# Kernel tuning notes

Measured on AMD Instinct MI355X. Metric: run time of the kernel, lower is better.

Reference implementation:

```python
import jax, jax.numpy as jnp
import numpy as np

B, C, T, H = 2, 1024, 2048, 16
D = C // H  # head dim = 64
SCALE = 1.0 / np.sqrt(D)
NEG_INF = jnp.float32(-1e30)


def setup_inputs() -> dict:
    key = jax.random.key(0)
    ks = jax.random.split(key, 10)
    x = jax.random.normal(ks[0], (B, C, T), dtype=jnp.float32)
    mask = jax.random.randint(ks[1], (B, 1, T), 0, 2).astype(bool)
    mask = mask.at[:, :, 0].set(True)  # avoid all-masked rows -> NaN softmax
    w = 1.0 / np.sqrt(C)
    Wq = jax.random.normal(ks[2], (C, C), dtype=jnp.float32) * w
    bq = jax.random.normal(ks[3], (C,), dtype=jnp.float32) * 0.01
    Wk = jax.random.normal(ks[4], (C, C), dtype=jnp.float32) * w
    bk = jax.random.normal(ks[5], (C,), dtype=jnp.float32) * 0.01
    Wv = jax.random.normal(ks[6], (C, C), dtype=jnp.float32) * w
    bv = jax.random.normal(ks[7], (C,), dtype=jnp.float32) * 0.01
    Wp = jax.random.normal(ks[8], (C, C), dtype=jnp.float32) * w
    bp = jax.random.normal(ks[9], (C,), dtype=jnp.float32) * 0.01
    return {"x": x, "mask": mask, "Wq": Wq, "bq": bq, "Wk": Wk, "bk": bk,
            "Wv": Wv, "bv": bv, "Wp": Wp, "bp": bp}


def _proj(W, b, x):
    # Conv1d with kernel_size=1: per-timestep linear on [B, C, T]
    return jnp.einsum('oc,bct->bot', W, x) + b[:, None]


def _heads(y):
    # [B, C, T] -> [B, H, T, D]
    return y.reshape(B, H, D, T).transpose(0, 1, 3, 2)


def reference(x, mask, Wq, bq, Wk, bk, Wv, bv, Wp, bp):
    q = _heads(_proj(Wq, bq, x))  # [B,H,T,D]
    k = _heads(_proj(Wk, bk, x))
    v = _heads(_proj(Wv, bv, x))
    att = jnp.einsum('bhqd,bhkd->bhqk', q * SCALE, k)  # [B,H,T,T]
    att = jnp.where(mask[:, :, None, :], att, NEG_INF)  # mask keys
    att = jax.nn.softmax(att, axis=-1)
    vm = v * mask[:, :, :, None].astype(v.dtype)  # zero masked values
    out = jnp.einsum('bhqk,bhkd->bhqd', att, vm)  # [B,H,T,D]
    out = out.transpose(0, 1, 3, 2).reshape(B, C, T)
    out = _proj(Wp, bp, out) * mask.astype(x.dtype)  # [B,C,T]
    return (out, mask)
```

## Files before the change

kernel.cpp:

```cpp
#include <hip/hip_runtime.h>
#include <hip/hip_bf16.h>
#include <math.h>

#define BB 2
#define CC 1024
#define TT 2048
#define HH 16
#define DD 64

using short8   = __attribute__((ext_vector_type(8))) short;
using floatx4  = __attribute__((ext_vector_type(4))) float;
using floatx16 = __attribute__((ext_vector_type(16))) float;
using uint2v   = __attribute__((ext_vector_type(2))) unsigned int;
typedef unsigned short ushort_t;

#define MFMA(a, b, c) __builtin_amdgcn_mfma_f32_16x16x32_bf16((a), (b), (c), 0, 0, 0)
#define MFMA32(a, b, c) __builtin_amdgcn_mfma_f32_32x32x16_bf16((a), (b), (c), 0, 0, 0)

#define QSC 0.18033688011112042f

#define PMAGIC   8404857.0f
#define PZERO_BF 0.97265625f

__device__ __forceinline__ ushort_t f2bf(float f) {
    unsigned int u = __float_as_uint(f);
    u += 0x7FFFu + ((u >> 16) & 1u);
    return (ushort_t)(u >> 16);
}
__device__ __forceinline__ float bf2f(ushort_t h) {
    return __uint_as_float(((unsigned int)h) << 16);
}
__device__ __forceinline__ ushort_t f2bf_t(float f) {
    return (ushort_t)(__float_as_uint(f) >> 16);
}
__device__ __forceinline__ unsigned int packtrunc(float a, float b) {
    return __builtin_amdgcn_perm(__float_as_uint(b), __float_as_uint(a),
                                 0x07060302u);
}
__device__ __forceinline__ unsigned int pack2bf_exp(float s0, float s1) {
    float f0 = fmaf(s0, 128.0f, PMAGIC);
    float f1 = fmaf(s1, 128.0f, PMAGIC);
    return __builtin_amdgcn_perm(__float_as_uint(f1), __float_as_uint(f0),
                                 0x05040100u);
}
__device__ __forceinline__ void load_lds16(const void* g, void* s) {
    __builtin_amdgcn_global_load_lds(
        (const __attribute__((address_space(1))) void*)g,
        (__attribute__((address_space(3))) void*)s, 16, 0, 0);
}

static constexpr size_t B0       = 65536;
static constexpr size_t XT_OFF   = B0;
static constexpr size_t WQKV_OFF = XT_OFF   + 8388608;
static constexpr size_t WP_OFF   = WQKV_OFF + 6291456;
static constexpr size_t Q_OFF    = WP_OFF   + 2097152;
static constexpr size_t K_OFF    = Q_OFF    + 8388608;
static constexpr size_t V_OFF    = K_OFF    + 8388608;
static constexpr size_t OP_OFF   = V_OFF    + 8388608;
static constexpr size_t ML_OFF   = OP_OFF   + 16777216;

__global__ __launch_bounds__(256) void prep_kernel(
    const float* __restrict__ x, const float* __restrict__ Wq,
    const float* __restrict__ Wk, const float* __restrict__ Wv,
    const float* __restrict__ Wp, const unsigned int* __restrict__ mraw,
    ushort_t* __restrict__ XT, ushort_t* __restrict__ WQKV,
    ushort_t* __restrict__ WP, float* __restrict__ maskf,
    int* __restrict__ nmcnt, float* __restrict__ out_tail) {
    __shared__ float tile[64][65];
    const int bid = blockIdx.x;
    const int tid = threadIdx.x;
    if (bid < 4096) {
        const int idx = bid * 256 + tid;
        if (idx < 786432) {
            int row = idx >> 8;
            int qc  = idx & 255;
            const float* src = row < 1024 ? Wq : (row < 2048 ? Wk : Wv);
            float4 v = *(const float4*)&src[(size_t)(row & 1023) * CC + qc * 4];
            ushort4 pk; pk.x = f2bf(v.x); pk.y = f2bf(v.y);
            pk.z = f2bf(v.z); pk.w = f2bf(v.w);
            *(ushort4*)&WQKV[(size_t)idx * 4] = pk;
        } else {
            int j = idx - 786432;
            float4 v = *(const float4*)&Wp[(size_t)j * 4];
            ushort4 pk; pk.x = f2bf(v.x); pk.y = f2bf(v.y);
            pk.z = f2bf(v.z); pk.w = f2bf(v.w);
            *(ushort4*)&WP[(size_t)j * 4] = pk;
        }
    } else if (bid < 5120) {
        const int xb = bid - 4096;
        const int t0 = (xb & 31) * 64, c0 = ((xb >> 5) & 15) * 64, b = xb >> 9;
        const int tc = tid & 15, tr = tid >> 4;
        #pragma unroll
        for (int p = 0; p < 4; p++) {
            int cl = tr + p * 16;
            float4 v = *(const float4*)&x[((size_t)b * CC + c0 + cl) * TT + t0 + tc * 4];
            tile[cl][tc * 4 + 0] = v.x; tile[cl][tc * 4 + 1] = v.y;
            tile[cl][tc * 4 + 2] = v.z; tile[cl][tc * 4 + 3] = v.w;
        }
        __syncthreads();
        #pragma unroll
        for (int p = 0; p < 4; p++) {
            int tl = tr + p * 16;
            ushort4 pk;
            pk.x = f2bf(tile[tc * 4 + 0][tl]);
            pk.y = f2bf(tile[tc * 4 + 1][tl]);
            pk.z = f2bf(tile[tc * 4 + 2][tl]);
            pk.w = f2bf(tile[tc * 4 + 3][tl]);
            *(ushort4*)&XT[((size_t)b * TT + t0 + tl) * CC + c0 + tc * 4] = pk;
        }
    } else {
        __shared__ int ev_bf16, ev_bool, cnt;
        const int mb = bid - 5120;
        if (tid == 0) { ev_bf16 = 0; ev_bool = 0; cnt = 0; }
        __syncthreads();
        for (int i = tid; i < 1024; i += 256) {
            unsigned int w = mraw[i];
            if ((w & 0xFFFFu) == 0x3F80u) atomicOr(&ev_bf16, 1);
            if ((w & 0xFFFFFF00u) != 0u && w != 0x3F800000u) atomicOr(&ev_bool, 1);
        }
        __syncthreads();
        const int mode = ev_bf16 ? 2 : (ev_bool ? 1 : 0);
        const int e = mb * 256 + tid;
        bool on;
        if (mode == 2)      on = ((const ushort_t*)mraw)[e] != 0;
        else if (mode == 1) on = ((const unsigned char*)mraw)[e] != 0;
        else                on = mraw[e] != 0;
        maskf[e]    = on ? 1.0f : 0.0f;
        out_tail[e] = on ? 1.0f : 0.0f;
        if (!on) atomicAdd(&cnt, 1);
        __syncthreads();
        if (tid == 0) nmcnt[mb] = cnt;
    }
}

__global__ __launch_bounds__(256) void gemm_qkv_kernel(
    const ushort_t* __restrict__ Wqkv, const float* __restrict__ bq,
    const float* __restrict__ bk, const float* __restrict__ bv,
    const ushort_t* __restrict__ XT, const float* __restrict__ maskf,
    ushort_t* __restrict__ Qo, ushort_t* __restrict__ Ko,
    ushort_t* __restrict__ Vo) {
    __shared__ ushort_t As[128][32];
    __shared__ ushort_t Bs[128][32];
    __shared__ float biasS[128];

    const int b = blockIdx.z;
    const int m0 = blockIdx.y * 128;
    const int n0 = blockIdx.x * 128;
    const int tid = threadIdx.x;
    const int lane = tid & 63;
    const int w = tid >> 6;
    const int wm = (w & 1) * 64, wn = (w >> 1) * 64;
    const int la = lane & 15, lg = lane >> 4;
    const int region = m0 >> 10;

    const float* bsrc = region == 0 ? (bq + m0)
                      : (region == 1 ? (bk + m0 - 1024) : (bv + m0 - 2048));
    if (tid < 128) biasS[tid] = bsrc[tid];

    float csc[4];
    #pragma unroll
    for (int nt = 0; nt < 4; nt++) {
        const int t = n0 + wn + nt * 16 + la;
        csc[nt] = (region == 0) ? QSC : maskf[b * TT + t];
    }

    floatx4 zero4 = {0.f, 0.f, 0.f, 0.f};
    floatx4 acc[4][4];
    #pragma unroll
    for (int mt = 0; mt < 4; mt++)
        #pragma unroll
        for (int nt = 0; nt < 4; nt++) acc[mt][nt] = zero4;

    const ushort_t* Abase = Wqkv + (size_t)m0 * CC;
    const ushort_t* Bbase = XT + ((size_t)b * TT + n0) * CC;
    const int rl = lane >> 2;
    const int cl = (lane & 3) * 8;

    for (int k0 = 0; k0 < CC; k0 += 32) {
        #pragma unroll
        for (int c = 0; c < 2; c++) {
            int row = w * 32 + c * 16;
            load_lds16(Abase + (size_t)(row + rl) * CC + k0 + cl, &As[row][0]);
            load_lds16(Bbase + (size_t)(row + rl) * CC + k0 + cl, &Bs[row][0]);
        }
        __syncthreads();
        short8 af[4], bf[4];
        #pragma unroll
        for (int mt = 0; mt < 4; mt++)
            af[mt] = *(const short8*)&As[wm + mt * 16 + la][lg * 8];
        #pragma unroll
        for (int nt = 0; nt < 4; nt++)
            bf[nt] = *(const short8*)&Bs[wn + nt * 16 + la][lg * 8];
        #pragma unroll
        for (int mt = 0; mt < 4; mt++)
            #pragma unroll
            for (int nt = 0; nt < 4; nt++)
                acc[mt][nt] = MFMA(af[mt], bf[nt], acc[mt][nt]);
        __syncthreads();
    }

    #pragma unroll
    for (int mt = 0; mt < 4; mt++) {
        const int lm = wm + mt * 16 + lg * 4;
        const int gm = m0 + lm;
        #pragma unroll
        for (int nt = 0; nt < 4; nt++) {
            const int t = n0 + wn + nt * 16 + la;
            const float sc = csc[nt];
            float v0 = (acc[mt][nt][0] + biasS[lm + 0]) * sc;
            float v1 = (acc[mt][nt][1] + biasS[lm + 1]) * sc;
            float v2 = (acc[mt][nt][2] + biasS[lm + 2]) * sc;
            float v3 = (acc[mt][nt][3] + biasS[lm + 3]) * sc;
            if (region < 2) {
                int mq = gm & 1023;
                int hh = mq >> 6, db = mq & 63;
                ushort_t* dst = (region == 0 ? Qo : Ko)
                              + (((size_t)b * HH + hh) * TT + t) * DD + db;
                uint2 pk;
                pk.x = packtrunc(v0, v1);
                pk.y = packtrunc(v2, v3);
                *(uint2*)dst = pk;
            } else {
                int c = gm & 1023;
                Vo[((size_t)b * CC + c + 0) * TT + t] = f2bf_t(v0);
                Vo[((size_t)b * CC + c + 1) * TT + t] = f2bf_t(v1);
                Vo[((size_t)b * CC + c + 2) * TT + t] = f2bf_t(v2);
                Vo[((size_t)b * CC + c + 3) * TT + t] = f2bf_t(v3);
            }
        }
    }
}

__global__ __launch_bounds__(256, 4) void attn_kernel(
    const ushort_t* __restrict__ Qg, const ushort_t* __restrict__ Kg,
    const ushort_t* __restrict__ Vg, const int* __restrict__ nmcnt,
    ushort_t* __restrict__ Opart, float* __restrict__ lbuf) {
    __shared__ __align__(16) char ldsbuf[32768];

    const int sp = blockIdx.z & 1, b = blockIdx.z >> 1;
    const int hh = blockIdx.y, t0 = blockIdx.x * 128;
    const int j0base = sp * (TT / 2);
    const int tid  = threadIdx.x;
    const int lane = tid & 63;
    const int w    = tid >> 6;
    const int ln31 = lane & 31;
    const int h    = lane >> 5;
    const size_t qkbase = ((size_t)b * HH + hh) * TT * DD;
    const size_t vbase  = ((size_t)b * CC + hh * DD) * TT;

    const int tq = t0 + w * 32 + ln31;
    short8 qreg[4];
    {
        const ushort_t* qp = Qg + qkbase + (size_t)tq * DD + h * 8;
        #pragma unroll
        for (int kc = 0; kc < 4; kc++)
            qreg[kc] = *(const short8*)(qp + kc * 16);
    }

    const int i3   = lane >> 3;
    const int swzb = ((lane & 7) ^ i3) << 4;
    const char* ks0 = (const char*)(Kg + qkbase + (size_t)(j0base + 16 * w + i3) * DD) + swzb;
    const char* vs0 = (const char*)(Vg + vbase + (size_t)(16 * w + i3) * TT + j0base) + swzb;
    char* kd = ldsbuf + 2 * w * 1024;
    char* vd = ldsbuf + 16384 + 2 * w * 1024;

    int ka[4];
    {
        const int kxor = (ln31 & 7) << 4;
        #pragma unroll
        for (int kc = 0; kc < 4; kc++)
            ka[kc] = ln31 * 128 + ((kc * 32 + h * 16) ^ kxor);
    }

    floatx16 zero16 = {0.f,0.f,0.f,0.f,0.f,0.f,0.f,0.f,
                       0.f,0.f,0.f,0.f,0.f,0.f,0.f,0.f};
    floatx16 oacc[2];
    oacc[0] = zero16; oacc[1] = zero16;
    floatx16 lacc = zero16;
    short8 ones8;
    #pragma unroll
    for (int i = 0; i < 8; i++) ones8[i] = (short)0x3F80;

    load_lds16(ks0,          kd);
    load_lds16(ks0 + 1024,   kd + 1024);
    load_lds16(vs0,          vd);
    load_lds16(vs0 + 32768,  vd + 1024);
    ks0 += 8192; vs0 += 128;
    __syncthreads();

    #pragma unroll 2
    for (int kt = 0; kt < 16; kt++) {
        const int pp = (kt & 1) * 8192;
        const int pn = 8192 - pp;
        if (kt < 15) {
            load_lds16(ks0,         kd + pn);
            load_lds16(ks0 + 1024,  kd + pn + 1024);
            load_lds16(vs0,         vd + pn);
            load_lds16(vs0 + 32768, vd + pn + 1024);
            ks0 += 8192; vs0 += 128;
        }

        floatx16 sacc[2];
        sacc[0] = zero16; sacc[1] = zero16;
        __builtin_amdgcn_s_setprio(1);
        #pragma unroll
        for (int kc = 0; kc < 4; kc++) {
            short8 kf0 = *(const short8*)(ldsbuf + ka[kc] + pp);
            short8 kf1 = *(const short8*)(ldsbuf + ka[kc] + pp + 4096);
            sacc[0] = MFMA32(kf0, qreg[kc], sacc[0]);
            sacc[1] = MFMA32(kf1, qreg[kc], sacc[1]);
        }
        __builtin_amdgcn_s_setprio(0);

        unsigned int pd[16];
        #pragma unroll
        for (int mt = 0; mt < 2; mt++)
            #pragma unroll
            for (int g = 0; g < 4; g++) {
                pd[mt * 8 + g * 2 + 0] =
                    pack2bf_exp(sacc[mt][g * 4 + 0], sacc[mt][g * 4 + 1]);
                pd[mt * 8 + g * 2 + 1] =
                    pack2bf_exp(sacc[mt][g * 4 + 2], sacc[mt][g * 4 + 3]);
            }

        __builtin_amdgcn_s_setprio(1);
        #pragma unroll
        for (int kc = 0; kc < 4; kc++) {
            const int base = (kc >> 1) * 8 + (kc & 1) * 4;
            uint2v r02 = __builtin_amdgcn_permlane32_swap(
                pd[base + 0], pd[base + 2], false, false);
            uint2v r13 = __builtin_amdgcn_permlane32_swap(
                pd[base + 1], pd[base + 3], false, false);
            int4 fi;
            fi.x = (int)r02[0];
            fi.y = (int)r13[0];
            fi.z = (int)r02[1];
            fi.w = (int)r13[1];
            short8 pf = *(short8*)&fi;
            lacc = MFMA32(ones8, pf, lacc);
            short8 vf0 = *(const short8*)(ldsbuf + ka[kc] + pp + 16384);
            short8 vf1 = *(const short8*)(ldsbuf + ka[kc] + pp + 16384 + 4096);
            oacc[0] = MFMA32(vf0, pf, oacc[0]);
            oacc[1] = MFMA32(vf1, pf, oacc[1]);
        }
        __builtin_amdgcn_s_setprio(0);

        if (kt < 15) __syncthreads();
    }

    float lsum = lacc[0];
    {
        const int r4 = (b * 2 + sp) * 4;
        int nm = nmcnt[r4] + nmcnt[r4 + 1] + nmcnt[r4 + 2] + nmcnt[r4 + 3];
        lsum -= (float)nm * PZERO_BF;
    }

    const float inv = lsum > 0.0f ? 1.0f / lsum : 0.0f;
    ushort_t* OP = Opart + (size_t)sp * ((size_t)BB * TT * CC)
                 + ((size_t)b * TT + tq) * CC + hh * 64;
    #pragma unroll
    for (int mt = 0; mt < 2; mt++)
        #pragma unroll
        for (int g = 0; g < 4; g++) {
            int db = mt * 32 + g * 8 + h * 4;
            ushort4 pk;
            pk.x = f2bf(oacc[mt][g * 4 + 0] * inv);
            pk.y = f2bf(oacc[mt][g * 4 + 1] * inv);
            pk.z = f2bf(oacc[mt][g * 4 + 2] * inv);
            pk.w = f2bf(oacc[mt][g * 4 + 3] * inv);
            *(ushort4*)&OP[db] = pk;
        }
    if (h == 0)
        lbuf[(((size_t)sp * BB + b) * HH + hh) * TT + tq] = lsum;
}

__global__ __launch_bounds__(256) void combine_kernel(
    const ushort_t* __restrict__ Opart, const float* __restrict__ lbuf,
    ushort_t* __restrict__ OT) {
    const size_t idx = ((size_t)blockIdx.x * 256 + threadIdx.x) * 8;
    const int c0 = (int)(idx & (CC - 1));
    const int t  = (int)((idx >> 10) & (TT - 1));
    const int b  = (int)(idx >> 21);
    const int hh = c0 >> 6;
    const float l0 = lbuf[(((size_t)0 * BB + b) * HH + hh) * TT + t];
    const float l1 = lbuf[(((size_t)1 * BB + b) * HH + hh) * TT + t];
    const float sum = l0 + l1;
    const float ws = sum > 0.0f ? 1.0f / sum : 0.0f;
    const float w0 = l0 * ws, w1 = l1 * ws;
    const ushort_t* P0 = Opart + idx;
    const ushort_t* P1 = Opart + (size_t)BB * TT * CC + idx;
    ushort4 a0 = *(const ushort4*)(P0);
    ushort4 a1 = *(const ushort4*)(P0 + 4);
    ushort4 b0 = *(const ushort4*)(P1);
    ushort4 b1 = *(const ushort4*)(P1 + 4);
    ushort4 o0, o1;
    o0.x = f2bf(w0 * bf2f(a0.x) + w1 * bf2f(b0.x));
    o0.y = f2bf(w0 * bf2f(a0.y) + w1 * bf2f(b0.y));
    o0.z = f2bf(w0 * bf2f(a0.z) + w1 * bf2f(b0.z));
    o0.w = f2bf(w0 * bf2f(a0.w) + w1 * bf2f(b0.w));
    o1.x = f2bf(w0 * bf2f(a1.x) + w1 * bf2f(b1.x));
    o1.y = f2bf(w0 * bf2f(a1.y) + w1 * bf2f(b1.y));
    o1.z = f2bf(w0 * bf2f(a1.z) + w1 * bf2f(b1.z));
    o1.w = f2bf(w0 * bf2f(a1.w) + w1 * bf2f(b1.w));
    *(ushort4*)&OT[idx]     = o0;
    *(ushort4*)&OT[idx + 4] = o1;
}

__global__ __launch_bounds__(256) void gemm_out_kernel(
    const ushort_t* __restrict__ WP, const ushort_t* __restrict__ OT,
    const float* __restrict__ bp, const float* __restrict__ maskf,
    float* __restrict__ out) {
    __shared__ ushort_t As[64][32];
    __shared__ ushort_t Bs[128][32];
    __shared__ float biasS[64];

    const int b = blockIdx.z;
    const int m0 = blockIdx.y * 64;
    const int n0 = blockIdx.x * 128;
    const int tid = threadIdx.x;
    const int lane = tid & 63;
    const int w = tid >> 6;
    const int wm = (w & 1) * 32, wn = (w >> 1) * 64;
    const int la = lane & 15, lg = lane >> 4;

    if (tid < 64) biasS[tid] = bp[m0 + tid];

    floatx4 zero4 = {0.f, 0.f, 0.f, 0.f};
    floatx4 acc[2][4];
    #pragma unroll
    for (int mt = 0; mt < 2; mt++)
        #pragma unroll
        for (int nt = 0; nt < 4; nt++) acc[mt][nt] = zero4;

    const int rl = lane >> 2;
    const int cl = (lane & 3) * 8;
    const ushort_t* Bbase = OT + ((size_t)b * TT + n0) * CC;

    for (int k0 = 0; k0 < CC; k0 += 32) {
        {
            int row = w * 16;
            load_lds16(WP + (size_t)(m0 + row + rl) * CC + k0 + cl, &As[row][0]);
        }
        #pragma unroll
        for (int c = 0; c < 2; c++) {
            int row = w * 32 + c * 16;
            load_lds16(Bbase + (size_t)(row + rl) * CC + k0 + cl, &Bs[row][0]);
        }
        __syncthreads();
        short8 af[2], bf[4];
        #pragma unroll
        for (int mt = 0; mt < 2; mt++)
            af[mt] = *(const short8*)&As[wm + mt * 16 + la][lg * 8];
        #pragma unroll
        for (int nt = 0; nt < 4; nt++)
            bf[nt] = *(const short8*)&Bs[wn + nt * 16 + la][lg * 8];
        #pragma unroll
        for (int mt = 0; mt < 2; mt++)
            #pragma unroll
            for (int nt = 0; nt < 4; nt++)
                acc[mt][nt] = MFMA(af[mt], bf[nt], acc[mt][nt]);
        __syncthreads();
    }

    #pragma unroll
    for (int mt = 0; mt < 2; mt++) {
        const int lm = wm + mt * 16 + lg * 4;
        #pragma unroll
        for (int nt = 0; nt < 4; nt++) {
            const int t = n0 + wn + nt * 16 + la;
            const float mk = maskf[b * TT + t];
            #pragma unroll
            for (int r = 0; r < 4; r++)
                out[((size_t)b * CC + m0 + lm + r) * TT + t] =
                    (acc[mt][nt][r] + biasS[lm + r]) * mk;
        }
    }
}

extern "C" void kernel_launch(void* const* d_in, const int* in_sizes, int n_in,
                              void* d_out, int out_size, void* d_ws,
                              size_t ws_size, hipStream_t stream) {
    const float* x    = (const float*)d_in[0];
    const void*  mask = d_in[1];
    const float* Wq   = (const float*)d_in[2];
    const float* bq   = (const float*)d_in[3];
    const float* Wk   = (const float*)d_in[4];
    const float* bk   = (const float*)d_in[5];
    const float* Wv   = (const float*)d_in[6];
    const float* bv   = (const float*)d_in[7];
    const float* Wp   = (const float*)d_in[8];
    const float* bp   = (const float*)d_in[9];

    float* out  = (float*)d_out;
    float* wsf  = (float*)d_ws;
    int* nmcnt  = (int*)d_ws + 16;
    float* maskf = wsf + 1024;
    char* wsb = (char*)d_ws;
    ushort_t* XT    = (ushort_t*)(wsb + XT_OFF);
    ushort_t* WQKV  = (ushort_t*)(wsb + WQKV_OFF);
    ushort_t* WPb   = (ushort_t*)(wsb + WP_OFF);
    ushort_t* Qb    = (ushort_t*)(wsb + Q_OFF);
    ushort_t* Kb    = (ushort_t*)(wsb + K_OFF);
    ushort_t* Vb    = (ushort_t*)(wsb + V_OFF);
    ushort_t* Opart = (ushort_t*)(wsb + OP_OFF);
    float*    lbuf  = (float*)(wsb + ML_OFF);

    prep_kernel<<<5136, 256, 0, stream>>>(x, Wq, Wk, Wv, Wp,
                                          (const unsigned int*)mask, XT, WQKV,
                                          WPb, maskf, nmcnt,
                                          out + (size_t)BB * CC * TT);

    gemm_qkv_kernel<<<dim3(TT / 128, 3 * CC / 128, BB), 256, 0, stream>>>(
        WQKV, bq, bk, bv, XT, maskf, Qb, Kb, Vb);

    attn_kernel<<<dim3(TT / 128, HH, BB * 2), 256, 0, stream>>>(
        Qb, Kb, Vb, nmcnt, Opart, lbuf);

    combine_kernel<<<2048, 256, 0, stream>>>(Opart, lbuf, XT);

    gemm_out_kernel<<<dim3(TT / 128, CC / 64, BB), 256, 0, stream>>>(
        WPb, XT, bp, maskf, out);
}
```

Baseline: 192.6 us.

## Remap attention grid for XCD-aware L2 reuse and switch LDS swizzle to rotation

The attention launch becomes a 1D grid of 1024 blocks, and the block index is decoded so that the 16 query tiles sharing one (batch, head, split) run on the same XCD. Those blocks reuse the same K/V in that XCD's L2 instead of spreading it across all eight. The LDS swizzle also changes from XOR to an additive rotation, applied consistently on the store and read sides, which alters the bank-conflict pattern. The remaining edits rename loop variables to avoid a clash with the new variable g.

```diff
diff --git a/kernel.cpp b/kernel.cpp
--- a/kernel.cpp
+++ b/kernel.cpp
@@ -237,8 +237,17 @@
     ushort_t* __restrict__ Opart, float* __restrict__ lbuf) {
     __shared__ __align__(16) char ldsbuf[32768];
 
-    const int sp = blockIdx.z & 1, b = blockIdx.z >> 1;
-    const int hh = blockIdx.y, t0 = blockIdx.x * 128;
+    const unsigned int bid = blockIdx.x;
+    const unsigned int xcd = bid & 7u;
+    const unsigned int rr  = bid >> 3;
+    const unsigned int x   = rr & 15u;
+    const unsigned int j   = rr >> 4;
+    const unsigned int g   = (j << 3) | xcd;
+    const int hh  = (int)(g & 15u);
+    const int z   = (int)(g >> 4);
+    const int sp  = z & 1, b = z >> 1;
+    const int t0  = (int)x * 128;
+
     const int j0base = sp * (TT / 2);
     const int tid  = threadIdx.x;
     const int lane = tid & 63;
@@ -258,19 +267,16 @@
     }
 
     const int i3   = lane >> 3;
-    const int swzb = ((lane & 7) ^ i3) << 4;
+    const int swzb = (((lane & 7) + 8 - i3) & 7) << 4;
     const char* ks0 = (const char*)(Kg + qkbase + (size_t)(j0base + 16 * w + i3) * DD) + swzb;
     const char* vs0 = (const char*)(Vg + vbase + (size_t)(16 * w + i3) * TT + j0base) + swzb;
     char* kd = ldsbuf + 2 * w * 1024;
     char* vd = ldsbuf + 16384 + 2 * w * 1024;
 
     int ka[4];
-    {
-        const int kxor = (ln31 & 7) << 4;
-        #pragma unroll
-        for (int kc = 0; kc < 4; kc++)
-            ka[kc] = ln31 * 128 + ((kc * 32 + h * 16) ^ kxor);
-    }
+    #pragma unroll
+    for (int kc = 0; kc < 4; kc++)
+        ka[kc] = ln31 * 128 + (((kc * 2 + h + ln31) & 7) << 4);
 
     floatx16 zero16 = {0.f,0.f,0.f,0.f,0.f,0.f,0.f,0.f,
                        0.f,0.f,0.f,0.f,0.f,0.f,0.f,0.f};
@@ -316,11 +322,11 @@
         #pragma unroll
         for (int mt = 0; mt < 2; mt++)
             #pragma unroll
-            for (int g = 0; g < 4; g++) {
-                pd[mt * 8 + g * 2 + 0] =
-                    pack2bf_exp(sacc[mt][g * 4 + 0], sacc[mt][g * 4 + 1]);
-                pd[mt * 8 + g * 2 + 1] =
-                    pack2bf_exp(sacc[mt][g * 4 + 2], sacc[mt][g * 4 + 3]);
+            for (int g2 = 0; g2 < 4; g2++) {
+                pd[mt * 8 + g2 * 2 + 0] =
+                    pack2bf_exp(sacc[mt][g2 * 4 + 0], sacc[mt][g2 * 4 + 1]);
+                pd[mt * 8 + g2 * 2 + 1] =
+                    pack2bf_exp(sacc[mt][g2 * 4 + 2], sacc[mt][g2 * 4 + 3]);
             }
 
         __builtin_amdgcn_s_setprio(1);
@@ -361,13 +367,13 @@
     #pragma unroll
     for (int mt = 0; mt < 2; mt++)
         #pragma unroll
-        for (int g = 0; g < 4; g++) {
-            int db = mt * 32 + g * 8 + h * 4;
+        for (int g2 = 0; g2 < 4; g2++) {
+            int db = mt * 32 + g2 * 8 + h * 4;
             ushort4 pk;
-            pk.x = f2bf(oacc[mt][g * 4 + 0] * inv);
-            pk.y = f2bf(oacc[mt][g * 4 + 1] * inv);
-            pk.z = f2bf(oacc[mt][g * 4 + 2] * inv);
-            pk.w = f2bf(oacc[mt][g * 4 + 3] * inv);
+            pk.x = f2bf(oacc[mt][g2 * 4 + 0] * inv);
+            pk.y = f2bf(oacc[mt][g2 * 4 + 1] * inv);
+            pk.z = f2bf(oacc[mt][g2 * 4 + 2] * inv);
+            pk.w = f2bf(oacc[mt][g2 * 4 + 3] * inv);
             *(ushort4*)&OP[db] = pk;
         }
     if (h == 0)
@@ -513,7 +519,7 @@
     gemm_qkv_kernel<<<dim3(TT / 128, 3 * CC / 128, BB), 256, 0, stream>>>(
         WQKV, bq, bk, bv, XT, maskf, Qb, Kb, Vb);
 
-    attn_kernel<<<dim3(TT / 128, HH, BB * 2), 256, 0, stream>>>(
+    attn_kernel<<<dim3(1024), 256, 0, stream>>>(
         Qb, Kb, Vb, nmcnt, Opart, lbuf);
 
     combine_kernel<<<2048, 256, 0, stream>>>(Opart, lbuf, XT);
```

New measurement: 192.0 us (median of 2 runs). No clear change (-0.3%).
